# Kernel tuning notes

Hardware: AMD Instinct MI355X
Metric: run time of the kernel (lower is better)

The kernel has to match this reference:

```python
import jax, jax.numpy as jnp
import numpy as np

D_MODEL = 768
NUM_HEADS = 12
HEAD_DIM = D_MODEL // NUM_HEADS
D_FF = 3072
LN_EPS = 1e-5


def _xavier(key, shape):
    # nn.init.xavier_uniform_ on a [out, in] Linear weight
    fan_out, fan_in = shape[-2], shape[-1]
    limit = float(np.sqrt(6.0 / (fan_in + fan_out)))
    return jax.random.uniform(key, shape, jnp.float32, -limit, limit)


def setup_inputs() -> dict:
    key = jax.random.key(0)
    ks = jax.random.split(key, 10)
    x = jax.random.normal(ks[0], (4, 2048, D_MODEL), jnp.float32)
    # per-head projections stacked: [H, head_dim, d_model] (torch Linear weight layout [out, in])
    Wq = _xavier(ks[1], (NUM_HEADS, HEAD_DIM, D_MODEL))
    Wk = _xavier(ks[2], (NUM_HEADS, HEAD_DIM, D_MODEL))
    Wv = _xavier(ks[3], (NUM_HEADS, HEAD_DIM, D_MODEL))
    Wo = _xavier(ks[4], (D_MODEL, D_MODEL))
    W1 = jax.random.normal(ks[5], (D_FF, D_MODEL), jnp.float32) * 0.02
    b1 = jnp.zeros((D_FF,), jnp.float32)
    W2 = jax.random.normal(ks[6], (D_MODEL, D_FF), jnp.float32) * 0.02
    b2 = jnp.zeros((D_MODEL,), jnp.float32)
    g1 = jnp.ones((D_MODEL,), jnp.float32)
    be1 = jnp.zeros((D_MODEL,), jnp.float32)
    g2 = jnp.ones((D_MODEL,), jnp.float32)
    be2 = jnp.zeros((D_MODEL,), jnp.float32)
    return {"x": x, "Wq": Wq, "Wk": Wk, "Wv": Wv, "Wo": Wo,
            "W1": W1, "b1": b1, "W2": W2, "b2": b2,
            "g1": g1, "be1": be1, "g2": g2, "be2": be2}


def _layernorm(x, g, b):
    mu = jnp.mean(x, axis=-1, keepdims=True)
    var = jnp.mean(jnp.square(x - mu), axis=-1, keepdims=True)
    return (x - mu) * jax.lax.rsqrt(var + LN_EPS) * g + b


def reference(x, Wq, Wk, Wv, Wo, W1, b1, W2, b2, g1, be1, g2, be2):
    B, S, D = x.shape
    # all heads batched (same math as the per-head Python loop + concat)
    q = jnp.einsum('bsd,hed->bhse', x, Wq)   # [B,H,S,e]
    k = jnp.einsum('bsd,hed->bhse', x, Wk)
    v = jnp.einsum('bsd,hed->bhse', x, Wv)
    scores = jnp.einsum('bhse,bhte->bhst', q, k) / jnp.sqrt(jnp.float32(HEAD_DIM))
    attn = jax.nn.softmax(scores, axis=-1)
    ctx = jnp.einsum('bhst,bhte->bhse', attn, v)
    # concat heads along feature dim (head order matches stacking order)
    concat = ctx.transpose(0, 2, 1, 3).reshape(B, S, D)
    attn_out = concat @ Wo.T
    h = _layernorm(x + attn_out, g1, be1)
    ffn = jax.nn.relu(h @ W1.T + b1) @ W2.T + b2
    out = _layernorm(h + ffn, g2, be2)
    return out
```

## Files before the change

kernel.cpp:

```cpp
#include <hip/hip_runtime.h>

typedef unsigned short u16;
typedef unsigned int u32;
typedef __attribute__((ext_vector_type(8))) short short8;
typedef __attribute__((ext_vector_type(4))) float f32x4;
typedef __attribute__((ext_vector_type(4))) unsigned short u16x4;

__device__ __forceinline__ float b2f(u16 u){
  union { float f; unsigned int i; } c; c.i = ((unsigned int)u) << 16; return c.f;
}
__device__ __forceinline__ u16 f2b(float f){
  union { float f; unsigned int i; } c; c.f = f;
  unsigned int i = c.i;
  unsigned int r = (i + 0x7FFFu + ((i >> 16) & 1u)) >> 16;
  return (u16)r;
}

#define EXP2(x) exp2f(x)

#define GLD16(gp, lp) __builtin_amdgcn_global_load_lds( \
    (const __attribute__((address_space(1))) void*)(gp), \
    (__attribute__((address_space(3))) void*)(lp), 16, 0, 0)

__device__ __forceinline__ u32 pkbf(float lo, float hi){
  u32 r;
  asm volatile("v_cvt_pk_bf16_f32 %0, %1, %2" : "=v"(r) : "v"(lo), "v"(hi));
  return r;
}

__global__ __launch_bounds__(256) void cvt_all(
    const float* __restrict__ s0, const float* __restrict__ s1,
    const float* __restrict__ s2, const float* __restrict__ s3,
    const float* __restrict__ s4, const float* __restrict__ s5,
    const float* __restrict__ s6, u16* __restrict__ dst)
{
  const int i = (blockIdx.x * 256 + threadIdx.x) * 4;
  const float* sp;
  if      (i <  6291456) sp = s0 + i;
  else if (i <  6881280) sp = s1 + (i - 6291456);
  else if (i <  7471104) sp = s2 + (i - 6881280);
  else if (i <  8060928) sp = s3 + (i - 7471104);
  else if (i <  8650752) sp = s4 + (i - 8060928);
  else if (i < 11010048) sp = s5 + (i - 8650752);
  else                   sp = s6 + (i - 11010048);
  float4 f = *(const float4*)sp;
  u16x4 o = { f2b(f.x), f2b(f.y), f2b(f.z), f2b(f.w) };
  *(u16x4*)(dst + i) = o;
}

__global__ __launch_bounds__(256) void transpose_v(const u16* __restrict__ v,
                                                   u16* __restrict__ vt){
  __shared__ short t[64][72];
  const int plane = blockIdx.y;
  const u16* vp = v + (size_t)plane * 2048 * 64;
  u16* vtp = vt + (size_t)plane * 2048 * 64;
  const int s0 = blockIdx.x * 64;
#pragma unroll
  for (int j = 0; j < 2; j++){
    int ch = threadIdx.x + 256*j;
    int r = ch >> 3, c = (ch & 7) << 3;
    short8 val = *(const short8*)(vp + (size_t)(s0 + r)*64 + c);
#pragma unroll
    for (int jj = 0; jj < 8; jj++) t[c + jj][r] = val[jj];
  }
  __syncthreads();
#pragma unroll
  for (int j = 0; j < 2; j++){
    int ch = threadIdx.x + 256*j;
    int r = ch >> 3, c = (ch & 7) << 3;
    *(short8*)(vtp + (size_t)r*2048 + s0 + c) = *(const short8*)&t[r][c];
  }
}

enum { EPI_QKV = 0, EPI_WO = 1, EPI_FFN1 = 2, EPI_FFN2 = 3 };
__device__ __forceinline__ float KSCALE_C(){ return 0.125f * 1.44269504088896340736f; }

template<int EPI>
__global__ __launch_bounds__(256) void gemm_bt(
    const u16* __restrict__ A, const u16* __restrict__ Bm,
    int K, int gx,
    u16* __restrict__ outB,
    const float* __restrict__ auxF,
    const u16* __restrict__ auxB)
{
  __shared__ __align__(16) short Asm[128][32];
  __shared__ __align__(16) short Bsm[128][32];
  const int tid  = threadIdx.x;
  const int lane = tid & 63;
  const int wid  = tid >> 6;
  const int wr = wid >> 1, wc = wid & 1;
  const int fr = lane & 15, fq = lane >> 4;

  const int nwg = gridDim.x;
  const int lin = blockIdx.x;
  const int wg  = (lin & 7) * (nwg >> 3) + (lin >> 3);
  const int bx = wg % gx, by = wg / gx;
  const int m0 = by * 128, n0 = bx * 128;

  f32x4 acc[4][4];
#pragma unroll
  for (int i = 0; i < 4; i++)
#pragma unroll
    for (int j = 0; j < 4; j++) acc[i][j] = (f32x4){0.f, 0.f, 0.f, 0.f};

  const int lrow = lane >> 2;
  const int lcol = (lane & 3) << 3;

  for (int k0 = 0; k0 < K; k0 += 32) {
    const u16* ga = A  + (size_t)(m0 + wid*32 + lrow) * K + k0 + lcol;
    const u16* gb = Bm + (size_t)(n0 + wid*32 + lrow) * K + k0 + lcol;
    GLD16(ga,                 &Asm[wid*32][0]);
    GLD16(ga + (size_t)16*K,  &Asm[wid*32 + 16][0]);
    GLD16(gb,                 &Bsm[wid*32][0]);
    GLD16(gb + (size_t)16*K,  &Bsm[wid*32 + 16][0]);
    __syncthreads();

    short8 a[4], b[4];
#pragma unroll
    for (int i = 0; i < 4; i++) a[i] = *(const short8*)&Asm[wr*64 + i*16 + fr][fq*8];
#pragma unroll
    for (int j = 0; j < 4; j++) b[j] = *(const short8*)&Bsm[wc*64 + j*16 + fr][fq*8];
    __builtin_amdgcn_s_setprio(1);
#pragma unroll
    for (int i = 0; i < 4; i++)
#pragma unroll
      for (int j = 0; j < 4; j++)
        acc[i][j] = __builtin_amdgcn_mfma_f32_16x16x32_bf16(a[i], b[j], acc[i][j], 0, 0, 0);
    __builtin_amdgcn_s_setprio(0);
    __syncthreads();
  }

#pragma unroll
  for (int i = 0; i < 4; i++) {
    const int row0 = m0 + wr*64 + i*16 + fq*4;
#pragma unroll
    for (int j = 0; j < 4; j++) {
      const int col = n0 + wc*64 + j*16 + fr;
#pragma unroll
      for (int r = 0; r < 4; r++) {
        const int row = row0 + r;
        float val = acc[i][j][r];
        if (EPI == EPI_QKV) {
          int tt = (col >= 1536) ? 2 : (col >= 768 ? 1 : 0);
          int rem = col - tt * 768;
          int h = rem >> 6, e = rem & 63;
          int bb = row >> 11, s = row & 2047;
          size_t idx = (((size_t)(tt*48 + bb*12 + h)) * 2048 + s) * 64 + e;
          if (tt == 1) val *= KSCALE_C();
          outB[idx] = f2b(val);
        } else if (EPI == EPI_WO) {
          size_t idx = (size_t)row * 768 + col;
          outB[idx] = f2b(val + b2f(auxB[idx]));
        } else if (EPI == EPI_FFN1) {
          float o = val + auxF[col];
          o = o > 0.f ? o : 0.f;
          outB[(size_t)row * 3072 + col] = f2b(o);
        } else {
          size_t idx = (size_t)row * 768 + col;
          outB[idx] = f2b(val + auxF[col] + b2f(auxB[idx]));
        }
      }
    }
  }
}

__global__ __launch_bounds__(512) void flash_attn(
    const u16* __restrict__ q, const u16* __restrict__ kmat, const u16* __restrict__ vtmat,
    u16* __restrict__ ctx)
{
  const int tid = threadIdx.x;
  const int lane = tid & 63, wid = tid >> 6;
  const int fr = lane & 15, fq = lane >> 4;
  const int orig = blockIdx.x;
  const int wg = (orig & 7) * 96 + (orig >> 3);
  const int qb = wg & 15;
  const int ph = wg >> 4;
  const size_t plane = (size_t)ph * 2048 * 64;
  const u16* qp  = q + plane;
  const u16* kp  = kmat + plane;
  const u16* vtp = vtmat + plane;

  __shared__ __align__(16) short Ksm[2][64][64];
  __shared__ __align__(16) short Vsm[2][64][64];

  const int qr0 = qb*128 + wid*16;
  const short8 aq0 = *(const short8*)(qp + (size_t)(qr0 + fr)*64 + fq*8);
  const short8 aq1 = *(const short8*)(qp + (size_t)(qr0 + fr)*64 + 32 + fq*8);

  short8 vones;
#pragma unroll
  for (int j = 0; j < 8; j++) vones[j] = (short)0x3F80;

  const int rA = wid*8 + (lane >> 3);
  const int cA = (((lane & 7) ^ ((rA & 3) | (((rA >> 3) & 1) << 2)))) * 8;

#define STAGE(B, KT) do { \
    GLD16(kp  + (size_t)((KT)*64 + rA)*64 + cA,  &Ksm[B][wid*8][0]); \
    GLD16(vtp + (size_t)rA*2048 + (KT)*64 + cA,  &Vsm[B][wid*8][0]); \
  } while(0)

  f32x4 o[4];
#pragma unroll
  for (int eb = 0; eb < 4; eb++) o[eb] = (f32x4){0.f, 0.f, 0.f, 0.f};
  float mneg = 0.f, l = 0.f;
  const f32x4 zero = (f32x4){0.f, 0.f, 0.f, 0.f};

  STAGE(0, 0);
  __syncthreads();

  const int fK  = (fr & 3) | (((fr >> 2) & 1) << 2);
  const int kc0 = ((fq    ) ^ fK) * 8;
  const int kc1 = ((4 + fq) ^ fK) * 8;
  const int krow = (fr & 3) + 8 * (fr >> 2);
  const int fV  = (fr & 3) | (((fr >> 3) & 1) << 2);
  const int vc0 = ((fq    ) ^ fV) * 8;
  const int vc1 = ((4 + fq) ^ fV) * 8;

  int buf = 0;
  for (int kt = 0; kt < 32; ++kt) {
    if (kt < 31) STAGE(buf ^ 1, kt + 1);

    f32x4 st[2][2];
    const f32x4 cini = (f32x4){mneg, mneg, mneg, mneg};
    __builtin_amdgcn_s_setprio(1);
#pragma unroll
    for (int h = 0; h < 2; h++)
#pragma unroll
      for (int c = 0; c < 2; c++) {
        const short* kr = &Ksm[buf][32*h + 4*c + krow][0];
        short8 kf0 = *(const short8*)(kr + kc0);
        short8 kf1 = *(const short8*)(kr + kc1);
        f32x4 a = __builtin_amdgcn_mfma_f32_16x16x32_bf16(kf0, aq0, cini, 0, 0, 0);
        st[h][c]  = __builtin_amdgcn_mfma_f32_16x16x32_bf16(kf1, aq1, a,    0, 0, 0);
      }
    __builtin_amdgcn_s_setprio(0);

    float t0 = fmaxf(fmaxf(st[0][0][0], st[0][0][1]), st[0][0][2]);
    float t1 = fmaxf(fmaxf(st[0][0][3], st[0][1][0]), st[0][1][1]);
    float t2 = fmaxf(fmaxf(st[0][1][2], st[0][1][3]), st[1][0][0]);
    float t3 = fmaxf(fmaxf(st[1][0][1], st[1][0][2]), st[1][0][3]);
    float t4 = fmaxf(fmaxf(st[1][1][0], st[1][1][1]), st[1][1][2]);
    float u0 = fmaxf(fmaxf(t0, t1), st[1][1][3]);
    float u1 = fmaxf(fmaxf(t2, t3), t4);
    float lm = fmaxf(u0, u1);
    lm = fmaxf(lm, __shfl_xor(lm, 16));
    lm = fmaxf(lm, __shfl_xor(lm, 32));

    float p[2][2][4];
    if (!__all(lm <= 8.f)) {
      float d = fmaxf(lm, 0.f);
      float corr = EXP2(-d);
      mneg -= d;
      l *= corr;
#pragma unroll
      for (int eb = 0; eb < 4; eb++)
#pragma unroll
        for (int r = 0; r < 4; r++) o[eb][r] *= corr;
#pragma unroll
      for (int h = 0; h < 2; h++)
#pragma unroll
        for (int c = 0; c < 2; c++)
#pragma unroll
          for (int r = 0; r < 4; r++)
            p[h][c][r] = EXP2(st[h][c][r] - d);
    } else {
#pragma unroll
      for (int h = 0; h < 2; h++)
#pragma unroll
        for (int c = 0; c < 2; c++)
#pragma unroll
          for (int r = 0; r < 4; r++)
            p[h][c][r] = EXP2(st[h][c][r]);
    }

    union { u32 u[4]; short8 s8; } pf0, pf1;
    pf0.u[0] = pkbf(p[0][0][0], p[0][0][1]);
    pf0.u[1] = pkbf(p[0][0][2], p[0][0][3]);
    pf0.u[2] = pkbf(p[0][1][0], p[0][1][1]);
    pf0.u[3] = pkbf(p[0][1][2], p[0][1][3]);
    pf1.u[0] = pkbf(p[1][0][0], p[1][0][1]);
    pf1.u[1] = pkbf(p[1][0][2], p[1][0][3]);
    pf1.u[2] = pkbf(p[1][1][0], p[1][1][1]);
    pf1.u[3] = pkbf(p[1][1][2], p[1][1][3]);

    __builtin_amdgcn_s_setprio(1);
    f32x4 ol = __builtin_amdgcn_mfma_f32_16x16x32_bf16(vones, pf0.s8, zero, 0, 0, 0);
    ol       = __builtin_amdgcn_mfma_f32_16x16x32_bf16(vones, pf1.s8, ol,   0, 0, 0);
#pragma unroll
    for (int eb = 0; eb < 4; eb++) {
      const short* vr = &Vsm[buf][eb*16 + fr][0];
      o[eb] = __builtin_amdgcn_mfma_f32_16x16x32_bf16(*(const short8*)(vr + vc0), pf0.s8, o[eb], 0, 0, 0);
      o[eb] = __builtin_amdgcn_mfma_f32_16x16x32_bf16(*(const short8*)(vr + vc1), pf1.s8, o[eb], 0, 0, 0);
    }
    __builtin_amdgcn_s_setprio(0);
    l += ol[0];

    __syncthreads();
    buf ^= 1;
  }
#undef STAGE

  const float inv = 1.0f / l;
  const int s = qr0 + fr;
  u16* cp = ctx + ((size_t)((ph/12)*2048 + s)) * 768 + (ph%12)*64;
#pragma unroll
  for (int eb = 0; eb < 4; eb++) {
    u16x4 w = { f2b(o[eb][0]*inv), f2b(o[eb][1]*inv), f2b(o[eb][2]*inv), f2b(o[eb][3]*inv) };
    *(u16x4*)(cp + eb*16 + fq*4) = w;
  }
}

template<int F32OUT>
__global__ __launch_bounds__(256) void ln_k(const u16* __restrict__ in,
    const float* __restrict__ g, const float* __restrict__ be, void* __restrict__ outp)
{
  const int lane = threadIdx.x & 63, wid = threadIdx.x >> 6;
  const int row = blockIdx.x * 4 + wid;
  const u16* p = in + (size_t)row * 768;
  float v[12];
  float s = 0.f, s2 = 0.f;
#pragma unroll
  for (int i = 0; i < 6; i++) {
    ushort2 uv = *(const ushort2*)(p + i*128 + lane*2);
    v[2*i]   = b2f(uv.x);
    v[2*i+1] = b2f(uv.y);
    s += v[2*i] + v[2*i+1];
    s2 += v[2*i]*v[2*i] + v[2*i+1]*v[2*i+1];
  }
#pragma unroll
  for (int msk = 1; msk < 64; msk <<= 1) { s += __shfl_xor(s, msk); s2 += __shfl_xor(s2, msk); }
  const float mu = s * (1.f/768.f);
  const float var = s2 * (1.f/768.f) - mu*mu;
  const float rstd = rsqrtf(var + 1e-5f);
#pragma unroll
  for (int i = 0; i < 6; i++) {
    int c = i*128 + lane*2;
    float o0 = (v[2*i]   - mu) * rstd * g[c]   + be[c];
    float o1 = (v[2*i+1] - mu) * rstd * g[c+1] + be[c+1];
    if (F32OUT) {
      float2 w = { o0, o1 };
      *(float2*)((float*)outp + (size_t)row*768 + c) = w;
    } else {
      ushort2 w = { f2b(o0), f2b(o1) };
      *(ushort2*)((u16*)outp + (size_t)row*768 + c) = w;
    }
  }
}

extern "C" void kernel_launch(void* const* d_in, const int* in_sizes, int n_in,
                              void* d_out, int out_size, void* d_ws, size_t ws_size,
                              hipStream_t stream)
{
  const float* x   = (const float*)d_in[0];
  const float* Wq  = (const float*)d_in[1];
  const float* Wk  = (const float*)d_in[2];
  const float* Wv  = (const float*)d_in[3];
  const float* Wo  = (const float*)d_in[4];
  const float* W1  = (const float*)d_in[5];
  const float* b1  = (const float*)d_in[6];
  const float* W2  = (const float*)d_in[7];
  const float* b2  = (const float*)d_in[8];
  const float* g1  = (const float*)d_in[9];
  const float* be1 = (const float*)d_in[10];
  const float* g2  = (const float*)d_in[11];
  const float* be2 = (const float*)d_in[12];
  float* out = (float*)d_out;

  char* ws = (char*)d_ws;
  u16* xb     = (u16*)(ws + 0);
  u16* Wqkv_b = (u16*)(ws + 12582912);
  u16* Wo_b   = (u16*)(ws + 16121856);
  u16* W1_b   = (u16*)(ws + 17301504);
  u16* W2_b   = (u16*)(ws + 22020096);
  u16* qkv    = (u16*)(ws + 26738688);
  u16* ctxb   = (u16*)(ws + 64487424);
  u16* hidden = (u16*)(ws + 26738688);
  u16* vt     = (u16*)(ws + 77070336);
  u16* resid1 = (u16*)(ws + 77070336);
  u16* hb     = (u16*)(ws + 102236160);
  u16* pre2   = (u16*)(ws + 77070336);

  cvt_all<<<dim3(13056), 256, 0, stream>>>(x, Wq, Wk, Wv, Wo, W1, W2, (u16*)ws);

  gemm_bt<EPI_QKV><<<dim3(1152), 256, 0, stream>>>(
      xb, Wqkv_b, 768, 18, qkv, nullptr, nullptr);

  u16* qb_ = qkv;
  u16* kb_ = qkv + 6291456;
  u16* vb_ = qkv + 12582912;

  transpose_v<<<dim3(32, 48), 256, 0, stream>>>(vb_, vt);

  flash_attn<<<dim3(768), 512, 0, stream>>>(qb_, kb_, vt, ctxb);

  gemm_bt<EPI_WO><<<dim3(384), 256, 0, stream>>>(
      ctxb, Wo_b, 768, 6, resid1, nullptr, xb);

  ln_k<0><<<2048, 256, 0, stream>>>(resid1, g1, be1, hb);

  gemm_bt<EPI_FFN1><<<dim3(1536), 256, 0, stream>>>(
      hb, W1_b, 768, 24, hidden, b1, nullptr);

  gemm_bt<EPI_FFN2><<<dim3(384), 256, 0, stream>>>(
      hidden, W2_b, 3072, 6, pre2, b2, hb);

  ln_k<1><<<2048, 256, 0, stream>>>(pre2, g2, be2, out);
}
```

Measured before the change: 321.2 us.

## Fuse V transpose into QKV GEMM epilogue and use native exp2 in attention

The QKV GEMM epilogue now writes V directly in transposed [plane][e][s] layout through the aux pointer, which removes the separate transpose_v kernel and its extra read and write of V. Flash attention switches to the native exp2 intrinsic. Its online softmax changes from a max folded into the MFMA accumulator init to an explicit running max m, subtracted before exp2 and rescaled lazily with an 8-unit threshold. The transposed V stores are strided by 2048 elements across lanes, so that epilogue writes are poorly coalesced, and the explicit subtraction adds VALU work per score element.

Result: faster. 302.6 us (-5.8%).

```diff
diff --git a/kernel.cpp b/kernel.cpp
--- a/kernel.cpp
+++ b/kernel.cpp
@@ -6,6 +6,9 @@
 typedef __attribute__((ext_vector_type(4))) float f32x4;
 typedef __attribute__((ext_vector_type(4))) unsigned short u16x4;
 
+extern "C" __device__ float __ocml_native_exp2_f32(float);
+#define EXP2(x) __ocml_native_exp2_f32(x)
+
 __device__ __forceinline__ float b2f(u16 u){
   union { float f; unsigned int i; } c; c.i = ((unsigned int)u) << 16; return c.f;
 }
@@ -15,8 +18,6 @@
   unsigned int r = (i + 0x7FFFu + ((i >> 16) & 1u)) >> 16;
   return (u16)r;
 }
-
-#define EXP2(x) exp2f(x)
 
 #define GLD16(gp, lp) __builtin_amdgcn_global_load_lds( \
     (const __attribute__((address_space(1))) void*)(gp), \
@@ -48,30 +49,6 @@
   *(u16x4*)(dst + i) = o;
 }
 
-__global__ __launch_bounds__(256) void transpose_v(const u16* __restrict__ v,
-                                                   u16* __restrict__ vt){
-  __shared__ short t[64][72];
-  const int plane = blockIdx.y;
-  const u16* vp = v + (size_t)plane * 2048 * 64;
-  u16* vtp = vt + (size_t)plane * 2048 * 64;
-  const int s0 = blockIdx.x * 64;
-#pragma unroll
-  for (int j = 0; j < 2; j++){
-    int ch = threadIdx.x + 256*j;
-    int r = ch >> 3, c = (ch & 7) << 3;
-    short8 val = *(const short8*)(vp + (size_t)(s0 + r)*64 + c);
-#pragma unroll
-    for (int jj = 0; jj < 8; jj++) t[c + jj][r] = val[jj];
-  }
-  __syncthreads();
-#pragma unroll
-  for (int j = 0; j < 2; j++){
-    int ch = threadIdx.x + 256*j;
-    int r = ch >> 3, c = (ch & 7) << 3;
-    *(short8*)(vtp + (size_t)r*2048 + s0 + c) = *(const short8*)&t[r][c];
-  }
-}
-
 enum { EPI_QKV = 0, EPI_WO = 1, EPI_FFN1 = 2, EPI_FFN2 = 3 };
 __device__ __forceinline__ float KSCALE_C(){ return 0.125f * 1.44269504088896340736f; }
 
@@ -145,9 +122,14 @@
           int rem = col - tt * 768;
           int h = rem >> 6, e = rem & 63;
           int bb = row >> 11, s = row & 2047;
-          size_t idx = (((size_t)(tt*48 + bb*12 + h)) * 2048 + s) * 64 + e;
-          if (tt == 1) val *= KSCALE_C();
-          outB[idx] = f2b(val);
+          if (tt == 2) {
+            size_t idx = (((size_t)(bb*12 + h)) * 64 + e) * 2048 + s;
+            ((u16*)auxB)[idx] = f2b(val);
+          } else {
+            size_t idx = (((size_t)(tt*48 + bb*12 + h)) * 2048 + s) * 64 + e;
+            if (tt == 1) val *= KSCALE_C();
+            outB[idx] = f2b(val);
+          }
         } else if (EPI == EPI_WO) {
           size_t idx = (size_t)row * 768 + col;
           outB[idx] = f2b(val + b2f(auxB[idx]));
@@ -202,7 +184,7 @@
   f32x4 o[4];
 #pragma unroll
   for (int eb = 0; eb < 4; eb++) o[eb] = (f32x4){0.f, 0.f, 0.f, 0.f};
-  float mneg = 0.f, l = 0.f;
+  float m = -1e30f, l = 0.f;
   const f32x4 zero = (f32x4){0.f, 0.f, 0.f, 0.f};
 
   STAGE(0, 0);
@@ -221,7 +203,6 @@
     if (kt < 31) STAGE(buf ^ 1, kt + 1);
 
     f32x4 st[2][2];
-    const f32x4 cini = (f32x4){mneg, mneg, mneg, mneg};
     __builtin_amdgcn_s_setprio(1);
 #pragma unroll
     for (int h = 0; h < 2; h++)
@@ -230,7 +211,7 @@
         const short* kr = &Ksm[buf][32*h + 4*c + krow][0];
         short8 kf0 = *(const short8*)(kr + kc0);
         short8 kf1 = *(const short8*)(kr + kc1);
-        f32x4 a = __builtin_amdgcn_mfma_f32_16x16x32_bf16(kf0, aq0, cini, 0, 0, 0);
+        f32x4 a = __builtin_amdgcn_mfma_f32_16x16x32_bf16(kf0, aq0, zero, 0, 0, 0);
         st[h][c]  = __builtin_amdgcn_mfma_f32_16x16x32_bf16(kf1, aq1, a,    0, 0, 0);
       }
     __builtin_amdgcn_s_setprio(0);
@@ -246,32 +227,25 @@
     lm = fmaxf(lm, __shfl_xor(lm, 16));
     lm = fmaxf(lm, __shfl_xor(lm, 32));
 
+    if (!__all(lm <= m + 8.f)) {
+      float nm = fmaxf(m, lm);
+      float corr = EXP2(m - nm);
+      m = nm;
+      l *= corr;
+#pragma unroll
+      for (int eb = 0; eb < 4; eb++)
+#pragma unroll
+        for (int r = 0; r < 4; r++) o[eb][r] *= corr;
+    }
+
     float p[2][2][4];
-    if (!__all(lm <= 8.f)) {
-      float d = fmaxf(lm, 0.f);
-      float corr = EXP2(-d);
-      mneg -= d;
-      l *= corr;
-#pragma unroll
-      for (int eb = 0; eb < 4; eb++)
-#pragma unroll
-        for (int r = 0; r < 4; r++) o[eb][r] *= corr;
-#pragma unroll
-      for (int h = 0; h < 2; h++)
-#pragma unroll
-        for (int c = 0; c < 2; c++)
-#pragma unroll
-          for (int r = 0; r < 4; r++)
-            p[h][c][r] = EXP2(st[h][c][r] - d);
-    } else {
-#pragma unroll
-      for (int h = 0; h < 2; h++)
-#pragma unroll
-        for (int c = 0; c < 2; c++)
-#pragma unroll
-          for (int r = 0; r < 4; r++)
-            p[h][c][r] = EXP2(st[h][c][r]);
-    }
+#pragma unroll
+    for (int h = 0; h < 2; h++)
+#pragma unroll
+      for (int c = 0; c < 2; c++)
+#pragma unroll
+        for (int r = 0; r < 4; r++)
+          p[h][c][r] = EXP2(st[h][c][r] - m);
 
     union { u32 u[4]; short8 s8; } pf0, pf1;
     pf0.u[0] = pkbf(p[0][0][0], p[0][0][1]);
@@ -383,13 +357,10 @@
   cvt_all<<<dim3(13056), 256, 0, stream>>>(x, Wq, Wk, Wv, Wo, W1, W2, (u16*)ws);
 
   gemm_bt<EPI_QKV><<<dim3(1152), 256, 0, stream>>>(
-      xb, Wqkv_b, 768, 18, qkv, nullptr, nullptr);
+      xb, Wqkv_b, 768, 18, qkv, nullptr, vt);
 
   u16* qb_ = qkv;
   u16* kb_ = qkv + 6291456;
-  u16* vb_ = qkv + 12582912;
-
-  transpose_v<<<dim3(32, 48), 256, 0, stream>>>(vb_, vt);
 
   flash_attn<<<dim3(768), 512, 0, stream>>>(qb_, kb_, vt, ctxb);
 
```
